# Performance work log

Hardware: AMD Instinct MI355X
Metric: run time of the kernel (lower is better)

The kernel has to match this reference:

```python
import jax, jax.numpy as jnp
import numpy as np

# Winograd F(4x4, 3x3) transform matrices (m=4, r=3, a=6)
B_T = jnp.array([[4.,0.,-5.,0.,1.,0.],
                 [0.,-4.,-4.,1.,1.,0.],
                 [0.,4.,-4.,-1.,1.,0.],
                 [0.,-2.,-1.,2.,1.,0.],
                 [0.,2.,-1.,-2.,1.,0.],
                 [0.,4.,0.,-5.,0.,1.]], dtype=jnp.float32)
G = jnp.array([[1/4.,0.,0.],
               [-1/6.,-1/6.,-1/6.],
               [-1/6.,1/6.,-1/6.],
               [1/24.,1/12.,1/6.],
               [1/24.,-1/12.,1/6.],
               [0.,0.,1.]], dtype=jnp.float32)
A_T = jnp.array([[1.,1.,1.,1.,1.,0.],
                 [0.,1.,-1.,2.,-2.,0.],
                 [0.,1.,1.,4.,4.,0.],
                 [0.,1.,-1.,8.,-8.,1.]], dtype=jnp.float32)

M_OUT, R_K, A_IN = 4, 3, 6  # output tile m, kernel r, input tile a = m+r-1


def setup_inputs() -> dict:
    key = jax.random.key(0)
    k1, k2 = jax.random.split(key)
    x = jax.random.normal(k1, (16, 64, 130, 130), dtype=jnp.float32)
    w = jax.random.normal(k2, (64, 64, 3, 3), dtype=jnp.float32) * 0.05
    return {"input": x, "weight": w}


def reference(input, weight):
    N, C, H, W = input.shape
    K = weight.shape[0]
    m, r, a = M_OUT, R_K, A_IN
    T = (H - r + 1) // m  # tiles per spatial dim (perfect tiling)

    # Filter transform: U[k,c] = G @ w[k,c] @ G^T  -> [K,C,a,a]
    U = jnp.einsum('ai,kcij,bj->kcab', G, weight, G)

    # Extract overlapping a x a input tiles with stride m: [N,C,T,a,T,a]
    idx = (jnp.arange(T) * m)[:, None] + jnp.arange(a)[None, :]  # [T,a]
    tiles = input[:, :, idx, :][:, :, :, :, idx]

    # Input transform: V = B^T @ tile @ B  -> [N,T,T,C,a,a]
    V = jnp.einsum('ai,nctisj,bj->ntscab', B_T, tiles, B_T)
    Vp = V.reshape(N * T * T, C, a, a)  # [P,C,a,a]

    # Elementwise (tile-domain) multiply + channel reduce: M[p,k] = sum_c U[k,c]*V[p,c]
    Mt = jnp.einsum('kcab,pcab->pkab', U, Vp)  # [P,K,a,a]

    # Output transform: Y_tile = A^T @ M @ A -> [P,K,m,m]
    Yt = jnp.einsum('ai,pkij,bj->pkab', A_T, Mt, A_T)

    out = T * m  # = H - r + 1
    Y = Yt.reshape(N, T, T, K, m, m).transpose(0, 3, 1, 4, 2, 5).reshape(N, K, out, out)
    return Y
```

## Files before the change

### kernel.cpp

```cpp
#include <hip/hip_runtime.h>


__constant__ float c_AT[24] = {
  1.f, 0.f, 0.f, 0.f,
  1.f, 1.f, 1.f, 1.f,
  1.f,-1.f, 1.f,-1.f,
  1.f, 2.f, 4.f, 8.f,
  1.f,-2.f, 4.f,-8.f,
  0.f, 0.f, 0.f, 1.f
};

__device__ __forceinline__ void gl2lds16(const float* g, float* l) {
  __builtin_amdgcn_global_load_lds((const __attribute__((address_space(1))) void*)g,
                                   (__attribute__((address_space(3))) void*)l, 16, 0, 0);
}

__global__ __launch_bounds__(256) void k_filter(const float* __restrict__ w,
                                                float* __restrict__ U) {
  int g = blockIdx.x * 256 + threadIdx.x;
  int k = g & 63;
  int c = g >> 6;
  const float* wp = w + (size_t)(k * 64 + c) * 9;
  float w00 = wp[0], w01 = wp[1], w02 = wp[2];
  float w10 = wp[3], w11 = wp[4], w12 = wp[5];
  float w20 = wp[6], w21 = wp[7], w22 = wp[8];
  const float G[6][3] = {
    {0.25f, 0.f, 0.f},
    {-1.f/6.f, -1.f/6.f, -1.f/6.f},
    {-1.f/6.f,  1.f/6.f, -1.f/6.f},
    {1.f/24.f,  1.f/12.f, 1.f/6.f},
    {1.f/24.f, -1.f/12.f, 1.f/6.f},
    {0.f, 0.f, 1.f}
  };
  float t[6][3];
#pragma unroll
  for (int a = 0; a < 6; ++a) {
    t[a][0] = G[a][0]*w00 + G[a][1]*w10 + G[a][2]*w20;
    t[a][1] = G[a][0]*w01 + G[a][1]*w11 + G[a][2]*w21;
    t[a][2] = G[a][0]*w02 + G[a][1]*w12 + G[a][2]*w22;
  }
#pragma unroll
  for (int a = 0; a < 6; ++a) {
#pragma unroll
    for (int b = 0; b < 6; ++b) {
      float u = G[b][0]*t[a][0] + G[b][1]*t[a][1] + G[b][2]*t[a][2];
      U[(size_t)(a*6+b)*4096 + c*64 + k] = u;
    }
  }
}

__global__ __launch_bounds__(256) void k_input(const float* __restrict__ x,
                                               float* __restrict__ V,
                                               int n0, int Pchunk) {
  __shared__ float Ls[34*134];
  const int tid  = threadIdx.x;
  const int bi   = blockIdx.x;
  const int band = bi & 3;
  const int c    = (bi >> 2) & 63;
  const int nl   = bi >> 8;
  const float* xp = x + (size_t)((n0 + nl) * 64 + c) * (130*130) + band * 32 * 130;
  for (int idx = tid; idx < 34*65; idx += 256) {
    int r  = idx / 65;
    int c2 = idx - r * 65;
    *(float2*)&Ls[r*134 + c2*2] = *(const float2*)(xp + r*130 + c2*2);
  }
  __syncthreads();
  const int tyl = tid >> 5;
  const int tx  = tid & 31;
  const int ty  = band * 8 + tyl;
  const int p   = (nl * 32 + ty) * 32 + tx;
  const float* bl = &Ls[(tyl*4)*134 + tx*4];
  float t1[6][6];
#pragma unroll
  for (int j = 0; j < 6; ++j) {
    float d0 = bl[0*134+j], d1 = bl[1*134+j], d2 = bl[2*134+j];
    float d3 = bl[3*134+j], d4 = bl[4*134+j], d5 = bl[5*134+j];
    t1[0][j] =  4.f*d0 - 5.f*d2 + d4;
    t1[1][j] = -4.f*d1 - 4.f*d2 + d3 + d4;
    t1[2][j] =  4.f*d1 - 4.f*d2 - d3 + d4;
    t1[3][j] = -2.f*d1 -     d2 + 2.f*d3 + d4;
    t1[4][j] =  2.f*d1 -     d2 - 2.f*d3 + d4;
    t1[5][j] =  4.f*d1 - 5.f*d3 + d5;
  }
  float* vb = V + (size_t)c * Pchunk + p;
  const size_t abs_ = (size_t)64 * Pchunk;
#pragma unroll
  for (int a = 0; a < 6; ++a) {
    float s0=t1[a][0], s1=t1[a][1], s2=t1[a][2], s3=t1[a][3], s4=t1[a][4], s5=t1[a][5];
    float v0 =  4.f*s0 - 5.f*s2 + s4;
    float v1 = -4.f*s1 - 4.f*s2 + s3 + s4;
    float v2 =  4.f*s1 - 4.f*s2 - s3 + s4;
    float v3 = -2.f*s1 -     s2 + 2.f*s3 + s4;
    float v4 =  2.f*s1 -     s2 - 2.f*s3 + s4;
    float v5 =  4.f*s1 - 5.f*s3 + s5;
    vb[(size_t)(a*6+0)*abs_] = v0;
    vb[(size_t)(a*6+1)*abs_] = v1;
    vb[(size_t)(a*6+2)*abs_] = v2;
    vb[(size_t)(a*6+3)*abs_] = v3;
    vb[(size_t)(a*6+4)*abs_] = v4;
    vb[(size_t)(a*6+5)*abs_] = v5;
  }
}

__global__ __launch_bounds__(256) void k_gemm2(const float* __restrict__ V,
                                               const float* __restrict__ U,
                                               float* __restrict__ M,
                                               int Pchunk, int nPB) {
  __shared__ float Vs[2][16*256];
  __shared__ float Us[2][16*64];
  const int tid  = threadIdx.x;
  const int lane = tid & 63;
  const int wv   = tid >> 6;
  const unsigned bx = blockIdx.x;
  const int ab = bx / (unsigned)nPB;
  const int pb = bx - ab * nPB;
  const int p0 = pb * 256;

  const float* Vab = V + (size_t)ab * 64 * Pchunk + p0;
  const float* Uab = U + (size_t)ab * 4096;

  auto stage = [&](int cc, int b) {
#pragma unroll
    for (int i = 0; i < 4; ++i) {
      int rl = wv * 4 + i;
      gl2lds16(Vab + (size_t)(cc * 16 + rl) * Pchunk + lane * 4, &Vs[b][rl * 256]);
    }
    gl2lds16(Uab + cc * 1024 + wv * 256 + lane * 4, &Us[b][wv * 256]);
  };

  stage(0, 0);

  const int pt = tid & 31;
  const int kt = tid >> 5;
  float acc[8][8];
#pragma unroll
  for (int ki = 0; ki < 8; ++ki)
#pragma unroll
    for (int pi = 0; pi < 8; ++pi) acc[ki][pi] = 0.f;

  __syncthreads();

#pragma unroll
  for (int cc = 0; cc < 4; ++cc) {
    const int b = cc & 1;
    if (cc < 3) stage(cc + 1, b ^ 1);
#pragma unroll 4
    for (int c = 0; c < 16; ++c) {
      const float4 va = *(const float4*)&Vs[b][c*256 + pt*4];
      const float4 vb = *(const float4*)&Vs[b][c*256 + 128 + pt*4];
      const float4 ua = *(const float4*)&Us[b][c*64 + kt*8];
      const float4 ub = *(const float4*)&Us[b][c*64 + kt*8 + 4];
      const float vv[8] = {va.x, va.y, va.z, va.w, vb.x, vb.y, vb.z, vb.w};
      const float uu[8] = {ua.x, ua.y, ua.z, ua.w, ub.x, ub.y, ub.z, ub.w};
#pragma unroll
      for (int ki = 0; ki < 8; ++ki)
#pragma unroll
        for (int pi = 0; pi < 8; ++pi)
          acc[ki][pi] += uu[ki] * vv[pi];
    }
    __syncthreads();
  }

#pragma unroll
  for (int ki = 0; ki < 8; ++ki) {
    float* mb = M + ((size_t)ab * 64 + kt*8 + ki) * Pchunk + p0;
    *(float4*)(mb + pt*4)       = make_float4(acc[ki][0], acc[ki][1], acc[ki][2], acc[ki][3]);
    *(float4*)(mb + 128 + pt*4) = make_float4(acc[ki][4], acc[ki][5], acc[ki][6], acc[ki][7]);
  }
}

__global__ __launch_bounds__(256) void k_out(const float* __restrict__ M,
                                             float* __restrict__ out,
                                             int n0, int Pchunk, int bpk) {
  const unsigned bx = blockIdx.x;
  const int k    = bx / (unsigned)bpk;
  const int pblk = bx - k * bpk;
  const int p    = pblk * 256 + threadIdx.x;
  const int nl = p >> 10;
  const int ty = (p >> 5) & 31;
  const int tx = p & 31;

  const float* mp = M + (size_t)k * Pchunk + p;
  const size_t abstride = (size_t)64 * Pchunk;
  float m[36];
#pragma unroll
  for (int ab = 0; ab < 36; ++ab) m[ab] = mp[(size_t)ab * abstride];

  float Y[4][4];
#pragma unroll
  for (int u = 0; u < 4; ++u)
#pragma unroll
    for (int v = 0; v < 4; ++v) Y[u][v] = 0.f;

#pragma unroll
  for (int i = 0; i < 6; ++i) {
    float R[4] = {0.f, 0.f, 0.f, 0.f};
#pragma unroll
    for (int j = 0; j < 6; ++j) {
      float mm = m[i*6 + j];
#pragma unroll
      for (int v = 0; v < 4; ++v) R[v] += c_AT[j*4 + v] * mm;
    }
#pragma unroll
    for (int u = 0; u < 4; ++u) {
      float au = c_AT[i*4 + u];
#pragma unroll
      for (int v = 0; v < 4; ++v) Y[u][v] += au * R[v];
    }
  }

  float* ob = out + ((size_t)((n0 + nl) * 64 + k) * 128 + ty*4) * 128 + tx*4;
#pragma unroll
  for (int u = 0; u < 4; ++u)
    *(float4*)(ob + (size_t)u * 128) = make_float4(Y[u][0], Y[u][1], Y[u][2], Y[u][3]);
}

extern "C" void kernel_launch(void* const* d_in, const int* in_sizes, int n_in,
                              void* d_out, int out_size, void* d_ws, size_t ws_size,
                              hipStream_t stream) {
  const float* x = (const float*)d_in[0];
  const float* w = (const float*)d_in[1];
  float* out = (float*)d_out;
  float* U = (float*)d_ws;
  const size_t U_bytes = 36ull * 64 * 64 * 4;
  const size_t per_n = 2ull * 36 * 1024 * 64 * 4;
  size_t avail = ws_size > U_bytes ? ws_size - U_bytes : 0;
  int chunk = 8;
  while (chunk > 1 && per_n * (size_t)chunk > avail) chunk >>= 1;
  if (per_n > avail) return;

  k_filter<<<16, 256, 0, stream>>>(w, U);
  for (int n0 = 0; n0 < 16; n0 += chunk) {
    int cn = (16 - n0) < chunk ? (16 - n0) : chunk;
    int Pchunk = cn * 1024;
    float* V = (float*)((char*)d_ws + U_bytes);
    float* M = V + (size_t)36 * 64 * Pchunk;
    int nPB = cn * 4;
    k_input<<<cn*256,  256, 0, stream>>>(x, V, n0, Pchunk);
    k_gemm2<<<36*nPB,  256, 0, stream>>>(V, U, M, Pchunk, nPB);
    k_out  <<<64*nPB,  256, 0, stream>>>(M, out, n0, Pchunk, nPB);
  }
}
```

Measured before the change: 261.9 us.

## Restructure batched GEMM: per-wave K slices with scalar U loads and triple-buffered V

Rewrites the tile-domain GEMM so each wave owns 16 output channels, and U is read through wave-uniform addresses that the compiler can turn into scalar loads, so U no longer passes through shared memory. V is staged in 8-channel slices across a three-deep LDS ring, with explicit vmcnt waits and raw barriers. The per-thread tile changes from 8x8 to 16x4, which lowers LDS traffic for U but means each V value is reused across fewer outputs per load. It relies on readfirstlane and hand-counted waitcnt values staying correct.

Result: slower. 729.6 us (+178.6%).

```diff
diff --git a/kernel.cpp b/kernel.cpp
--- a/kernel.cpp
+++ b/kernel.cpp
@@ -106,10 +106,9 @@
                                                const float* __restrict__ U,
                                                float* __restrict__ M,
                                                int Pchunk, int nPB) {
-  __shared__ float Vs[2][16*256];
-  __shared__ float Us[2][16*64];
+  __shared__ float Vs3[3][8*256];
   const int tid  = threadIdx.x;
-  const int lane = tid & 63;
+  const int ln   = tid & 63;
   const int wv   = tid >> 6;
   const unsigned bx = blockIdx.x;
   const int ab = bx / (unsigned)nPB;
@@ -117,55 +116,57 @@
   const int p0 = pb * 256;
 
   const float* Vab = V + (size_t)ab * 64 * Pchunk + p0;
-  const float* Uab = U + (size_t)ab * 4096;
-
-  auto stage = [&](int cc, int b) {
-#pragma unroll
-    for (int i = 0; i < 4; ++i) {
-      int rl = wv * 4 + i;
-      gl2lds16(Vab + (size_t)(cc * 16 + rl) * Pchunk + lane * 4, &Vs[b][rl * 256]);
-    }
-    gl2lds16(Uab + cc * 1024 + wv * 256 + lane * 4, &Us[b][wv * 256]);
+  const int klo = __builtin_amdgcn_readfirstlane(wv << 4);
+  const float* __restrict__ Uw = U + (size_t)ab * 4096 + klo;
+
+  auto stageV = [&](int cc, float* dst) {
+#pragma unroll
+    for (int i = 0; i < 2; ++i) {
+      int rl = wv * 2 + i;
+      gl2lds16(Vab + (size_t)(cc * 8 + rl) * Pchunk + ln * 4, dst + rl * 256);
+    }
   };
 
-  stage(0, 0);
-
-  const int pt = tid & 31;
-  const int kt = tid >> 5;
-  float acc[8][8];
-#pragma unroll
-  for (int ki = 0; ki < 8; ++ki)
-#pragma unroll
-    for (int pi = 0; pi < 8; ++pi) acc[ki][pi] = 0.f;
-
-  __syncthreads();
-
-#pragma unroll
-  for (int cc = 0; cc < 4; ++cc) {
-    const int b = cc & 1;
-    if (cc < 3) stage(cc + 1, b ^ 1);
-#pragma unroll 4
-    for (int c = 0; c < 16; ++c) {
-      const float4 va = *(const float4*)&Vs[b][c*256 + pt*4];
-      const float4 vb = *(const float4*)&Vs[b][c*256 + 128 + pt*4];
-      const float4 ua = *(const float4*)&Us[b][c*64 + kt*8];
-      const float4 ub = *(const float4*)&Us[b][c*64 + kt*8 + 4];
-      const float vv[8] = {va.x, va.y, va.z, va.w, vb.x, vb.y, vb.z, vb.w};
-      const float uu[8] = {ua.x, ua.y, ua.z, ua.w, ub.x, ub.y, ub.z, ub.w};
-#pragma unroll
-      for (int ki = 0; ki < 8; ++ki)
-#pragma unroll
-        for (int pi = 0; pi < 8; ++pi)
-          acc[ki][pi] += uu[ki] * vv[pi];
-    }
-    __syncthreads();
-  }
-
-#pragma unroll
-  for (int ki = 0; ki < 8; ++ki) {
-    float* mb = M + ((size_t)ab * 64 + kt*8 + ki) * Pchunk + p0;
-    *(float4*)(mb + pt*4)       = make_float4(acc[ki][0], acc[ki][1], acc[ki][2], acc[ki][3]);
-    *(float4*)(mb + 128 + pt*4) = make_float4(acc[ki][4], acc[ki][5], acc[ki][6], acc[ki][7]);
+  float acc[16][4];
+#pragma unroll
+  for (int ki = 0; ki < 16; ++ki)
+#pragma unroll
+    for (int pi = 0; pi < 4; ++pi) acc[ki][pi] = 0.f;
+
+  stageV(0, Vs3[0]);
+  stageV(1, Vs3[1]);
+
+#pragma unroll
+  for (int cc = 0; cc < 8; ++cc) {
+    if (cc < 7) { asm volatile("s_waitcnt vmcnt(2)" ::: "memory"); }
+    else        { asm volatile("s_waitcnt vmcnt(0)" ::: "memory"); }
+    __builtin_amdgcn_sched_barrier(0);
+    __builtin_amdgcn_s_barrier();
+    __builtin_amdgcn_sched_barrier(0);
+    if (cc < 6) stageV(cc + 2, Vs3[(cc + 2) % 3]);
+
+    const float* vbuf = Vs3[cc % 3];
+#pragma unroll
+    for (int cl = 0; cl < 8; ++cl) {
+      const float4 v4 = *(const float4*)&vbuf[cl * 256 + ln * 4];
+      const float* up = Uw + (size_t)(cc * 8 + cl) * 64;
+      float u[16];
+#pragma unroll
+      for (int ki = 0; ki < 16; ++ki) u[ki] = up[ki];
+#pragma unroll
+      for (int ki = 0; ki < 16; ++ki) {
+        acc[ki][0] += u[ki] * v4.x;
+        acc[ki][1] += u[ki] * v4.y;
+        acc[ki][2] += u[ki] * v4.z;
+        acc[ki][3] += u[ki] * v4.w;
+      }
+    }
+  }
+
+#pragma unroll
+  for (int ki = 0; ki < 16; ++ki) {
+    float* mb = M + ((size_t)ab * 64 + klo + ki) * Pchunk + p0;
+    *(float4*)(mb + ln * 4) = make_float4(acc[ki][0], acc[ki][1], acc[ki][2], acc[ki][3]);
   }
 }
 
```
